# Kernel optimization log

Measured on AMD Instinct MI355X. Metric: run time of the kernel, lower is better.

## Reference

```python
import jax, jax.numpy as jnp
import numpy as np
import math

EPS = 1e-5  # torch BatchNorm2d default eps
EXPANSION_RATE = 2


def _bn_train(x, gamma, beta):
    # BatchNorm2d in training mode: biased batch statistics over (B, H, W)
    mu = jnp.mean(x, axis=(0, 2, 3), keepdims=True)
    var = jnp.var(x, axis=(0, 2, 3), keepdims=True)
    xn = (x - mu) * jax.lax.rsqrt(var + EPS)
    return gamma[None, :, None, None] * xn + beta[None, :, None, None]


def _conv1x1(x, w, b):
    # w: [O, C]  (1x1 conv kernel squeezed), b: [O]
    return jnp.einsum('bchw,oc->bohw', x, w) + b[None, :, None, None]


def _lsgc(x, w_diff, b_diff, g_bn, be_bn, w_in, b_in, g_ibn, be_ibn,
          w_mr, b_mr, g_mbn, be_mbn):
    B, C, H, W = x.shape
    bit_depth = max(math.ceil(math.log2(H)), math.ceil(math.log2(W)))
    steps = [EXPANSION_RATE * 2 ** (n - 1) for n in range(1, bit_depth + 1)]

    fmax = None
    for step in steps:
        for axis, size in ((3, W), (2, H)):
            s = step % size
            for sgn in (1, -1):  # forward / backward rolls
                shifted = jnp.roll(x, sgn * s, axis=axis) if s else x
                d = x - shifted
                fmax = d if fmax is None else jnp.maximum(fmax, d)

    x_diff = _bn_train(_conv1x1(fmax, w_diff, b_diff), g_bn, be_bn)
    x_proc = _bn_train(_conv1x1(x, w_in, b_in), g_ibn, be_ibn)

    # MRConv: concat -> 1x1 conv -> BN -> GELU (exact) -> residual add
    x_cat = jnp.concatenate([x_proc, x_diff], axis=1)
    h = _bn_train(_conv1x1(x_cat, w_mr, b_mr), g_mbn, be_mbn)
    h = jax.nn.gelu(h, approximate=False)
    return x_proc + h


def setup_inputs() -> dict:
    key = jax.random.key(0)
    ks = jax.random.split(key, 8)
    B, C_in, C_out, H, W = 32, 128, 128, 64, 64

    def kaiming(k, o, i):
        return jax.random.normal(k, (o, i), jnp.float32) * np.sqrt(2.0 / i)

    return {
        'x': jax.random.normal(ks[0], (B, C_in, H, W), jnp.float32),
        'w_diff': kaiming(ks[1], C_out, C_in),
        'b_diff': jnp.zeros((C_out,), jnp.float32),
        'g_bn': jnp.ones((C_out,), jnp.float32),
        'be_bn': jnp.zeros((C_out,), jnp.float32),
        'w_in': kaiming(ks[2], C_out, C_in),
        'b_in': jnp.zeros((C_out,), jnp.float32),
        'g_ibn': jnp.ones((C_out,), jnp.float32),
        'be_ibn': jnp.zeros((C_out,), jnp.float32),
        'w_mr': kaiming(ks[3], C_out, 2 * C_out),
        'b_mr': jnp.zeros((C_out,), jnp.float32),
        'g_mbn': jnp.ones((C_out,), jnp.float32),
        'be_mbn': jnp.zeros((C_out,), jnp.float32),
    }


def reference(x, w_diff, b_diff, g_bn, be_bn, w_in, b_in, g_ibn, be_ibn,
              w_mr, b_mr, g_mbn, be_mbn):
    return _lsgc(x, w_diff, b_diff, g_bn, be_bn, w_in, b_in, g_ibn, be_ibn,
                 w_mr, b_mr, g_mbn, be_mbn)
```

## Files before the change

### kernel.cpp

```cpp
#include <hip/hip_runtime.h>
#include <math.h>


#define INV_NPIX (1.0f / 131072.0f)
#define EPS 1e-5f
#define KP 66

typedef __attribute__((ext_vector_type(8))) short s16x8;
typedef __attribute__((ext_vector_type(4))) float f32x4;

__device__ __forceinline__ uint32_t bf16_rne(float v) {
  uint32_t x = __float_as_uint(v);
  return (x + 0x7fffu + ((x >> 16) & 1u)) >> 16;
}
__device__ __forceinline__ uint32_t pack_hl(float v) {
  uint32_t h = bf16_rne(v);
  float lo = v - __uint_as_float(h << 16);
  return h | (bf16_rne(lo) << 16);
}

__device__ __forceinline__ float4 fmin4(float4 a, float4 b) {
  return make_float4(fminf(a.x, b.x), fminf(a.y, b.y), fminf(a.z, b.z),
                     fminf(a.w, b.w));
}

__global__ __launch_bounds__(256) void stencil_prep_kernel(
    const float* __restrict__ x, float* __restrict__ out,
    const float* __restrict__ w_in, const float* __restrict__ w_diff,
    unsigned short* __restrict__ wInH, unsigned short* __restrict__ wInL,
    unsigned short* __restrict__ wDfH, unsigned short* __restrict__ wDfL,
    float* __restrict__ stats) {
  __shared__ float4 p4[1024];
  if (blockIdx.x >= 4096) {
    const int t = (blockIdx.x - 4096) * 256 + threadIdx.x;
    if (t < 24576) stats[t] = 0.f;
    const int e = t & 16383;
    const float* w = (t < 16384) ? w_in : w_diff;
    unsigned short* aH = (t < 16384) ? wInH : wDfH;
    unsigned short* aL = (t < 16384) ? wInL : wDfL;
    const int j = e & 7, l = (e >> 3) & 63, mt = (e >> 9) & 7, kc = e >> 12;
    const int m = mt * 16 + (l & 15);
    const int k = kc * 32 + ((l >> 4) << 3) + j;
    const uint32_t p = pack_hl(w[m * 128 + k]);
    aH[e] = (unsigned short)(p & 0xffffu);
    aL[e] = (unsigned short)(p >> 16);
    return;
  }
  const size_t base4 = (size_t)blockIdx.x * 1024;
  float4 self[4];
#pragma unroll
  for (int i = 0; i < 4; ++i) {
    const int u = threadIdx.x + i * 256;
    self[i] = ((const float4*)x)[base4 + u];
    p4[u] = self[i];
  }
  __syncthreads();
#pragma unroll
  for (int i = 0; i < 4; ++i) {
    const int u = threadIdx.x + i * 256;
    const int h = u >> 4, wu = u & 15;
    const int row = u & ~15;
    const float4 A = self[i];
    const float4 L = p4[row | ((wu + 15) & 15)];
    const float4 R = p4[row | ((wu + 1) & 15)];
    float4 m = A;
    m = fmin4(m, L);
    m = fmin4(m, R);
    m = fmin4(m, make_float4(A.z, A.w, R.x, R.y));
    m = fmin4(m, make_float4(L.z, L.w, A.x, A.y));
    m = fmin4(m, p4[row | ((wu + 2) & 15)]);
    m = fmin4(m, p4[row | ((wu + 14) & 15)]);
    m = fmin4(m, p4[row | ((wu + 4) & 15)]);
    m = fmin4(m, p4[row | ((wu + 12) & 15)]);
    m = fmin4(m, p4[row | ((wu + 8) & 15)]);
    m = fmin4(m, p4[(((h + 2) & 63) << 4) | wu]);
    m = fmin4(m, p4[(((h + 62) & 63) << 4) | wu]);
    m = fmin4(m, p4[(((h + 4) & 63) << 4) | wu]);
    m = fmin4(m, p4[(((h + 60) & 63) << 4) | wu]);
    m = fmin4(m, p4[(((h + 8) & 63) << 4) | wu]);
    m = fmin4(m, p4[(((h + 56) & 63) << 4) | wu]);
    m = fmin4(m, p4[(((h + 16) & 63) << 4) | wu]);
    m = fmin4(m, p4[(((h + 48) & 63) << 4) | wu]);
    m = fmin4(m, p4[(((h + 32) & 63) << 4) | wu]);
    float4 o;
    o.x = A.x - m.x;
    o.y = A.y - m.y;
    o.z = A.z - m.z;
    o.w = A.w - m.w;
    ((float4*)out)[base4 + u] = o;
  }
}

template <int K>
__device__ __forceinline__ void gemm_body(
    const unsigned short* __restrict__ AH, const unsigned short* __restrict__ AL,
    const float* __restrict__ B0, const float* __restrict__ B1,
    float* __restrict__ out, float* __restrict__ sumv,
    float* __restrict__ sumq, const int bx, uint32_t* Bs) {
  const int tid = threadIdx.x;
  const int lane = tid & 63;
  const int wave = tid >> 6;
  const int b = bx >> 6;
  const int hw0 = (bx & 63) << 6;
  const int sn4 = tid & 15;
  const int sk = tid >> 4;
  const int q = lane >> 4;
  const int ln = lane & 15;
  constexpr int NC = K / 32;

  f32x4 acc[2][4];
#pragma unroll
  for (int i = 0; i < 2; ++i)
#pragma unroll
    for (int j = 0; j < 4; ++j) acc[i][j] = (f32x4)(0.0f);

  float4 ld[4][2];
#pragma unroll
  for (int c = 0; c < 4; ++c) {
#pragma unroll
    for (int s = 0; s < 2; ++s) {
      const int kr = sk + s * 16;
      ld[c][s] = *(const float4*)&B0[((size_t)b * 128 + c * 32 + kr) * 4096 +
                                     hw0 + (sn4 << 2)];
    }
  }

#pragma unroll
  for (int kc = 0; kc < NC; ++kc) {
    const int slot = kc & 3;
    const int bsel = kc & 1;
    uint32_t* buf = Bs + bsel * (32 * KP);
#pragma unroll
    for (int s = 0; s < 2; ++s) {
      const int kr = sk + s * 16;
      uint2 d01, d23;
      d01.x = pack_hl(ld[slot][s].x);
      d01.y = pack_hl(ld[slot][s].y);
      d23.x = pack_hl(ld[slot][s].z);
      d23.y = pack_hl(ld[slot][s].w);
      *(uint2*)&buf[kr * KP + (sn4 << 2)] = d01;
      *(uint2*)&buf[kr * KP + (sn4 << 2) + 2] = d23;
    }
    s16x8 ah[2], al[2];
#pragma unroll
    for (int mt2 = 0; mt2 < 2; ++mt2) {
      const size_t off = ((size_t)((kc * 8 + wave * 2 + mt2) * 64 + lane)) << 3;
      ah[mt2] = *(const s16x8*)(AH + off);
      al[mt2] = *(const s16x8*)(AL + off);
    }
    if (K == 256 && kc < 4) {
#pragma unroll
      for (int s = 0; s < 2; ++s) {
        const int kr = sk + s * 16;
        ld[slot][s] = *(const float4*)&B1[((size_t)b * 128 + kc * 32 + kr) *
                                              4096 + hw0 + (sn4 << 2)];
      }
    }
    __syncthreads();
#pragma unroll
    for (int nt = 0; nt < 4; ++nt) {
      uint32_t dj[8];
#pragma unroll
      for (int j = 0; j < 8; ++j) dj[j] = buf[(q * 8 + j) * KP + nt * 16 + ln];
      union { uint32_t u[4]; s16x8 s; } bh, bl;
#pragma unroll
      for (int jj = 0; jj < 4; ++jj) {
        bh.u[jj] = __builtin_amdgcn_perm(dj[2 * jj + 1], dj[2 * jj], 0x05040100u);
        bl.u[jj] = __builtin_amdgcn_perm(dj[2 * jj + 1], dj[2 * jj], 0x07060302u);
      }
#pragma unroll
      for (int mt2 = 0; mt2 < 2; ++mt2) {
        acc[mt2][nt] = __builtin_amdgcn_mfma_f32_16x16x32_bf16(
            ah[mt2], bh.s, acc[mt2][nt], 0, 0, 0);
        acc[mt2][nt] = __builtin_amdgcn_mfma_f32_16x16x32_bf16(
            ah[mt2], bl.s, acc[mt2][nt], 0, 0, 0);
        acc[mt2][nt] = __builtin_amdgcn_mfma_f32_16x16x32_bf16(
            al[mt2], bh.s, acc[mt2][nt], 0, 0, 0);
      }
    }
  }

  const int cb = (bx & 31) * 128;
#pragma unroll
  for (int mt2 = 0; mt2 < 2; ++mt2) {
    float sa[4] = {0.f, 0.f, 0.f, 0.f};
    float sq[4] = {0.f, 0.f, 0.f, 0.f};
#pragma unroll
    for (int nt = 0; nt < 4; ++nt) {
#pragma unroll
      for (int r = 0; r < 4; ++r) {
        const float v = acc[mt2][nt][r];
        const int m = (wave * 2 + mt2) * 16 + q * 4 + r;
        out[((size_t)b * 128 + m) * 4096 + hw0 + nt * 16 + ln] = v;
        sa[r] += v;
        sq[r] += v * v;
      }
    }
#pragma unroll
    for (int off = 1; off < 16; off <<= 1) {
#pragma unroll
      for (int r = 0; r < 4; ++r) {
        sa[r] += __shfl_xor(sa[r], off);
        sq[r] += __shfl_xor(sq[r], off);
      }
    }
    if (ln == 0) {
#pragma unroll
      for (int r = 0; r < 4; ++r) {
        const int m = (wave * 2 + mt2) * 16 + q * 4 + r;
        atomicAdd(&sumv[cb + m], sa[r]);
        atomicAdd(&sumq[cb + m], sq[r]);
      }
    }
  }
}

__global__ __launch_bounds__(256) void gemm1_dual(
    const unsigned short* __restrict__ AH1, const unsigned short* __restrict__ AL1,
    const float* __restrict__ X, float* __restrict__ out1,
    float* __restrict__ sv1, float* __restrict__ sq1,
    const unsigned short* __restrict__ AH2, const unsigned short* __restrict__ AL2,
    const float* __restrict__ F, float* __restrict__ out2,
    float* __restrict__ sv2, float* __restrict__ sq2) {
  __shared__ uint32_t Bs[2 * 32 * KP];
  const int bx = blockIdx.x & 2047;
  if ((blockIdx.x >> 11) == 0)
    gemm_body<128>(AH1, AL1, X, nullptr, out1, sv1, sq1, bx, Bs);
  else
    gemm_body<128>(AH2, AL2, F, nullptr, out2, sv2, sq2, bx, Bs);
}

__global__ __launch_bounds__(256) void gemm2_kernel(
    const unsigned short* __restrict__ AH, const unsigned short* __restrict__ AL,
    const float* __restrict__ B0, const float* __restrict__ B1,
    float* __restrict__ out, float* __restrict__ sv, float* __restrict__ sq) {
  __shared__ uint32_t Bs[2 * 32 * KP];
  gemm_body<256>(AH, AL, B0, B1, out, sv, sq, blockIdx.x, Bs);
}

__global__ __launch_bounds__(256) void finalize1_kernel(
    const float* __restrict__ pSin, const float* __restrict__ pQin,
    const float* __restrict__ pSdf, const float* __restrict__ pQdf,
    const float* __restrict__ g_ibn, const float* __restrict__ be_ibn,
    const float* __restrict__ g_bn, const float* __restrict__ w_mr,
    float* __restrict__ a_in, float* __restrict__ d_in,
    unsigned short* __restrict__ wEffH, unsigned short* __restrict__ wEffL) {
  __shared__ float sa[256];
  const int t = threadIdx.x;
  if (t < 128) {
    float s = 0.f, qq = 0.f;
#pragma unroll
    for (int i = 0; i < 32; ++i) {
      s += pSin[i * 128 + t];
      qq += pQin[i * 128 + t];
    }
    const float mu = s * INV_NPIX;
    const float var = fmaxf(qq * INV_NPIX - mu * mu, 0.f);
    const float a = g_ibn[t] * rsqrtf(var + EPS);
    if (blockIdx.x == 0) {
      a_in[t] = a;
      d_in[t] = be_ibn[t] - mu * a;
    }
    sa[t] = a;
  } else {
    const int c = t - 128;
    float s = 0.f, qq = 0.f;
#pragma unroll
    for (int i = 0; i < 32; ++i) {
      s += pSdf[i * 128 + c];
      qq += pQdf[i * 128 + c];
    }
    const float mu = s * INV_NPIX;
    const float var = fmaxf(qq * INV_NPIX - mu * mu, 0.f);
    sa[t] = g_bn[c] * rsqrtf(var + EPS);
  }
  __syncthreads();
  const int e = blockIdx.x * 256 + t;
  const int j = e & 7, l = (e >> 3) & 63, mt = (e >> 9) & 7, kc = e >> 12;
  const int m = mt * 16 + (l & 15);
  const int k = kc * 32 + ((l >> 4) << 3) + j;
  const uint32_t p = pack_hl(w_mr[m * 256 + k] * sa[k]);
  wEffH[e] = (unsigned short)(p & 0xffffu);
  wEffL[e] = (unsigned short)(p >> 16);
}

__global__ __launch_bounds__(128) void finalize2_kernel(
    const float* __restrict__ pSh, const float* __restrict__ pQh,
    const float* __restrict__ g_mbn, const float* __restrict__ be_mbn,
    float* __restrict__ a_m, float* __restrict__ d_m) {
  const int t = threadIdx.x;
  float s = 0.f, qq = 0.f;
#pragma unroll
  for (int i = 0; i < 32; ++i) {
    s += pSh[i * 128 + t];
    qq += pQh[i * 128 + t];
  }
  const float mu = s * INV_NPIX;
  const float var = fmaxf(qq * INV_NPIX - mu * mu, 0.f);
  const float a = g_mbn[t] * rsqrtf(var + EPS);
  a_m[t] = a;
  d_m[t] = be_mbn[t] - mu * a;
}

__device__ __forceinline__ float gelu_exact(float z) {
  return 0.5f * z * (1.0f + erff(z * 0.70710678118654752f));
}

__global__ __launch_bounds__(256) void epilogue_kernel(
    const float* __restrict__ y_in, const float* __restrict__ h_pre,
    const float* __restrict__ a_in, const float* __restrict__ d_in,
    const float* __restrict__ a_m, const float* __restrict__ d_m,
    float* __restrict__ out) {
  const size_t i = (size_t)blockIdx.x * 256 + threadIdx.x;
  const int c = (int)((i >> 10) & 127);
  const float4 y = ((const float4*)y_in)[i];
  const float4 h = ((const float4*)h_pre)[i];
  const float ai = a_in[c], di = d_in[c], am = a_m[c], dm = d_m[c];
  float4 o;
  o.x = fmaf(ai, y.x, di) + gelu_exact(fmaf(am, h.x, dm));
  o.y = fmaf(ai, y.y, di) + gelu_exact(fmaf(am, h.y, dm));
  o.z = fmaf(ai, y.z, di) + gelu_exact(fmaf(am, h.z, dm));
  o.w = fmaf(ai, y.w, di) + gelu_exact(fmaf(am, h.w, dm));
  ((float4*)out)[i] = o;
}

extern "C" void kernel_launch(void* const* d_in, const int* in_sizes, int n_in,
                              void* d_out, int out_size, void* d_ws,
                              size_t ws_size, hipStream_t stream) {
  const float* x = (const float*)d_in[0];
  const float* w_diff = (const float*)d_in[1];
  const float* g_bn = (const float*)d_in[3];
  const float* w_in = (const float*)d_in[5];
  const float* g_ibn = (const float*)d_in[7];
  const float* be_ibn = (const float*)d_in[8];
  const float* w_mr = (const float*)d_in[9];
  const float* g_mbn = (const float*)d_in[11];
  const float* be_mbn = (const float*)d_in[12];
  float* out = (float*)d_out;

  const size_t NB = (size_t)16777216;
  float* ws = (float*)d_ws;
  float* buf0 = ws;
  float* buf1 = ws + NB;
  float* buf2 = ws + 2 * NB;
  float* st = ws + 3 * NB;
  float* pSin = st, *pQin = st + 4096;
  float* pSdf = st + 8192, *pQdf = st + 12288;
  float* pSh = st + 16384, *pQh = st + 20480;
  float* a_in = st + 24576, *dinc = st + 24704;
  float* a_m = st + 24832, *d_m = st + 24960;
  unsigned short* fr = (unsigned short*)(st + 25088);
  unsigned short* wInH = fr;
  unsigned short* wInL = fr + 16384;
  unsigned short* wDfH = fr + 32768;
  unsigned short* wDfL = fr + 49152;
  unsigned short* wEffH = fr + 65536;
  unsigned short* wEffL = fr + 98304;

  stencil_prep_kernel<<<4224, 256, 0, stream>>>(x, buf0, w_in, w_diff, wInH,
                                                wInL, wDfH, wDfL, st);
  gemm1_dual<<<4096, 256, 0, stream>>>(wInH, wInL, x, buf1, pSin, pQin, wDfH,
                                       wDfL, buf0, buf2, pSdf, pQdf);
  finalize1_kernel<<<128, 256, 0, stream>>>(pSin, pQin, pSdf, pQdf, g_ibn,
                                            be_ibn, g_bn, w_mr, a_in, dinc,
                                            wEffH, wEffL);
  gemm2_kernel<<<2048, 256, 0, stream>>>(wEffH, wEffL, buf1, buf2, buf0, pSh,
                                         pQh);
  finalize2_kernel<<<1, 128, 0, stream>>>(pSh, pQh, g_mbn, be_mbn, a_m, d_m);
  epilogue_kernel<<<16384, 256, 0, stream>>>(buf1, buf0, a_in, dinc, a_m, d_m,
                                             out);
}
```

Measured before the change: 276.6 us.

## Store intermediates as channel-pair-packed bf16 and drop the low-part B split

The stencil kernel now emits x and the diff map as single bf16 values, with two channels packed per 32-bit word. The GEMMs read these packed operands straight into LDS without the hi/lo split, so each step issues 2 MFMAs instead of 3. GEMM outputs and the epilogue inputs are also stored in the same packed bf16 form, which roughly halves intermediate HBM traffic. In exchange the activations lose precision (a single bf16 instead of a hi+lo pair), which risks accuracy against the fp32 reference.

```diff
diff --git a/kernel.cpp b/kernel.cpp
--- a/kernel.cpp
+++ b/kernel.cpp
@@ -18,21 +18,27 @@
   float lo = v - __uint_as_float(h << 16);
   return h | (bf16_rne(lo) << 16);
 }
-
+__device__ __forceinline__ float bf_lo(uint32_t d) {
+  return __uint_as_float(d << 16);
+}
+__device__ __forceinline__ float bf_hi(uint32_t d) {
+  return __uint_as_float(d & 0xffff0000u);
+}
 __device__ __forceinline__ float4 fmin4(float4 a, float4 b) {
   return make_float4(fminf(a.x, b.x), fminf(a.y, b.y), fminf(a.z, b.z),
                      fminf(a.w, b.w));
 }
 
 __global__ __launch_bounds__(256) void stencil_prep_kernel(
-    const float* __restrict__ x, float* __restrict__ out,
-    const float* __restrict__ w_in, const float* __restrict__ w_diff,
-    unsigned short* __restrict__ wInH, unsigned short* __restrict__ wInL,
-    unsigned short* __restrict__ wDfH, unsigned short* __restrict__ wDfL,
-    float* __restrict__ stats) {
-  __shared__ float4 p4[1024];
-  if (blockIdx.x >= 4096) {
-    const int t = (blockIdx.x - 4096) * 256 + threadIdx.x;
+    const float* __restrict__ x, uint32_t* __restrict__ xp,
+    uint32_t* __restrict__ fp, const float* __restrict__ w_in,
+    const float* __restrict__ w_diff, unsigned short* __restrict__ wInH,
+    unsigned short* __restrict__ wInL, unsigned short* __restrict__ wDfH,
+    unsigned short* __restrict__ wDfL, float* __restrict__ stats) {
+  __shared__ float4 pA[1024];
+  __shared__ float4 pB[1024];
+  if (blockIdx.x >= 2048) {
+    const int t = (blockIdx.x - 2048) * 256 + threadIdx.x;
     if (t < 24576) stats[t] = 0.f;
     const int e = t & 16383;
     const float* w = (t < 16384) ? w_in : w_diff;
@@ -46,67 +52,102 @@
     aL[e] = (unsigned short)(p >> 16);
     return;
   }
-  const size_t base4 = (size_t)blockIdx.x * 1024;
-  float4 self[4];
+  const int b = blockIdx.x >> 6;
+  const int cp = blockIdx.x & 63;
+  const float4* xa = (const float4*)x + (size_t)(b * 128 + 2 * cp) * 1024;
+  const float4* xb = xa + 1024;
+  float4 sA[4], sB[4];
 #pragma unroll
   for (int i = 0; i < 4; ++i) {
     const int u = threadIdx.x + i * 256;
-    self[i] = ((const float4*)x)[base4 + u];
-    p4[u] = self[i];
+    sA[i] = xa[u];
+    sB[i] = xb[u];
+    pA[u] = sA[i];
+    pB[u] = sB[i];
   }
   __syncthreads();
+  const size_t obase = (size_t)(b * 64 + cp) * 1024;
 #pragma unroll
   for (int i = 0; i < 4; ++i) {
     const int u = threadIdx.x + i * 256;
     const int h = u >> 4, wu = u & 15;
     const int row = u & ~15;
-    const float4 A = self[i];
-    const float4 L = p4[row | ((wu + 15) & 15)];
-    const float4 R = p4[row | ((wu + 1) & 15)];
-    float4 m = A;
-    m = fmin4(m, L);
-    m = fmin4(m, R);
-    m = fmin4(m, make_float4(A.z, A.w, R.x, R.y));
-    m = fmin4(m, make_float4(L.z, L.w, A.x, A.y));
-    m = fmin4(m, p4[row | ((wu + 2) & 15)]);
-    m = fmin4(m, p4[row | ((wu + 14) & 15)]);
-    m = fmin4(m, p4[row | ((wu + 4) & 15)]);
-    m = fmin4(m, p4[row | ((wu + 12) & 15)]);
-    m = fmin4(m, p4[row | ((wu + 8) & 15)]);
-    m = fmin4(m, p4[(((h + 2) & 63) << 4) | wu]);
-    m = fmin4(m, p4[(((h + 62) & 63) << 4) | wu]);
-    m = fmin4(m, p4[(((h + 4) & 63) << 4) | wu]);
-    m = fmin4(m, p4[(((h + 60) & 63) << 4) | wu]);
-    m = fmin4(m, p4[(((h + 8) & 63) << 4) | wu]);
-    m = fmin4(m, p4[(((h + 56) & 63) << 4) | wu]);
-    m = fmin4(m, p4[(((h + 16) & 63) << 4) | wu]);
-    m = fmin4(m, p4[(((h + 48) & 63) << 4) | wu]);
-    m = fmin4(m, p4[(((h + 32) & 63) << 4) | wu]);
-    float4 o;
-    o.x = A.x - m.x;
-    o.y = A.y - m.y;
-    o.z = A.z - m.z;
-    o.w = A.w - m.w;
-    ((float4*)out)[base4 + u] = o;
-  }
-}
-
-template <int K>
+    float4 mA, mB;
+    {
+      const float4 A = sA[i];
+      const float4 L = pA[row | ((wu + 15) & 15)];
+      const float4 R = pA[row | ((wu + 1) & 15)];
+      float4 m = fmin4(A, fmin4(L, R));
+      m = fmin4(m, make_float4(A.z, A.w, R.x, R.y));
+      m = fmin4(m, make_float4(L.z, L.w, A.x, A.y));
+      m = fmin4(m, pA[row | ((wu + 2) & 15)]);
+      m = fmin4(m, pA[row | ((wu + 14) & 15)]);
+      m = fmin4(m, pA[row | ((wu + 4) & 15)]);
+      m = fmin4(m, pA[row | ((wu + 12) & 15)]);
+      m = fmin4(m, pA[row | ((wu + 8) & 15)]);
+      m = fmin4(m, pA[(((h + 2) & 63) << 4) | wu]);
+      m = fmin4(m, pA[(((h + 62) & 63) << 4) | wu]);
+      m = fmin4(m, pA[(((h + 4) & 63) << 4) | wu]);
+      m = fmin4(m, pA[(((h + 60) & 63) << 4) | wu]);
+      m = fmin4(m, pA[(((h + 8) & 63) << 4) | wu]);
+      m = fmin4(m, pA[(((h + 56) & 63) << 4) | wu]);
+      m = fmin4(m, pA[(((h + 16) & 63) << 4) | wu]);
+      m = fmin4(m, pA[(((h + 48) & 63) << 4) | wu]);
+      m = fmin4(m, pA[(((h + 32) & 63) << 4) | wu]);
+      mA = m;
+    }
+    {
+      const float4 A = sB[i];
+      const float4 L = pB[row | ((wu + 15) & 15)];
+      const float4 R = pB[row | ((wu + 1) & 15)];
+      float4 m = fmin4(A, fmin4(L, R));
+      m = fmin4(m, make_float4(A.z, A.w, R.x, R.y));
+      m = fmin4(m, make_float4(L.z, L.w, A.x, A.y));
+      m = fmin4(m, pB[row | ((wu + 2) & 15)]);
+      m = fmin4(m, pB[row | ((wu + 14) & 15)]);
+      m = fmin4(m, pB[row | ((wu + 4) & 15)]);
+      m = fmin4(m, pB[row | ((wu + 12) & 15)]);
+      m = fmin4(m, pB[row | ((wu + 8) & 15)]);
+      m = fmin4(m, pB[(((h + 2) & 63) << 4) | wu]);
+      m = fmin4(m, pB[(((h + 62) & 63) << 4) | wu]);
+      m = fmin4(m, pB[(((h + 4) & 63) << 4) | wu]);
+      m = fmin4(m, pB[(((h + 60) & 63) << 4) | wu]);
+      m = fmin4(m, pB[(((h + 8) & 63) << 4) | wu]);
+      m = fmin4(m, pB[(((h + 56) & 63) << 4) | wu]);
+      m = fmin4(m, pB[(((h + 16) & 63) << 4) | wu]);
+      m = fmin4(m, pB[(((h + 48) & 63) << 4) | wu]);
+      m = fmin4(m, pB[(((h + 32) & 63) << 4) | wu]);
+      mB = m;
+    }
+    uint4 px, pf;
+    px.x = bf16_rne(sA[i].x) | (bf16_rne(sB[i].x) << 16);
+    px.y = bf16_rne(sA[i].y) | (bf16_rne(sB[i].y) << 16);
+    px.z = bf16_rne(sA[i].z) | (bf16_rne(sB[i].z) << 16);
+    px.w = bf16_rne(sA[i].w) | (bf16_rne(sB[i].w) << 16);
+    pf.x = bf16_rne(sA[i].x - mA.x) | (bf16_rne(sB[i].x - mB.x) << 16);
+    pf.y = bf16_rne(sA[i].y - mA.y) | (bf16_rne(sB[i].y - mB.y) << 16);
+    pf.z = bf16_rne(sA[i].z - mA.z) | (bf16_rne(sB[i].z - mB.z) << 16);
+    pf.w = bf16_rne(sA[i].w - mA.w) | (bf16_rne(sB[i].w - mB.w) << 16);
+    ((uint4*)xp)[obase + u] = px;
+    ((uint4*)fp)[obase + u] = pf;
+  }
+}
+
+template <int NC>
 __device__ __forceinline__ void gemm_body(
     const unsigned short* __restrict__ AH, const unsigned short* __restrict__ AL,
-    const float* __restrict__ B0, const float* __restrict__ B1,
-    float* __restrict__ out, float* __restrict__ sumv,
+    const uint32_t* __restrict__ B0, const uint32_t* __restrict__ B1,
+    uint32_t* __restrict__ outp, float* __restrict__ sumv,
     float* __restrict__ sumq, const int bx, uint32_t* Bs) {
   const int tid = threadIdx.x;
   const int lane = tid & 63;
   const int wave = tid >> 6;
   const int b = bx >> 6;
   const int hw0 = (bx & 63) << 6;
-  const int sn4 = tid & 15;
-  const int sk = tid >> 4;
+  const int sk2 = tid >> 4;
+  const int sn4 = (tid & 15) << 2;
   const int q = lane >> 4;
   const int ln = lane & 15;
-  constexpr int NC = K / 32;
 
   f32x4 acc[2][4];
 #pragma unroll
@@ -114,33 +155,17 @@
 #pragma unroll
     for (int j = 0; j < 4; ++j) acc[i][j] = (f32x4)(0.0f);
 
-  float4 ld[4][2];
-#pragma unroll
-  for (int c = 0; c < 4; ++c) {
-#pragma unroll
-    for (int s = 0; s < 2; ++s) {
-      const int kr = sk + s * 16;
-      ld[c][s] = *(const float4*)&B0[((size_t)b * 128 + c * 32 + kr) * 4096 +
-                                     hw0 + (sn4 << 2)];
-    }
-  }
+  uint4 ld[4];
+#pragma unroll
+  for (int c = 0; c < 4; ++c)
+    ld[c] = *(const uint4*)&B0[((size_t)(b * 64 + c * 16 + sk2)) * 4096 + hw0 +
+                               sn4];
 
 #pragma unroll
   for (int kc = 0; kc < NC; ++kc) {
     const int slot = kc & 3;
-    const int bsel = kc & 1;
-    uint32_t* buf = Bs + bsel * (32 * KP);
-#pragma unroll
-    for (int s = 0; s < 2; ++s) {
-      const int kr = sk + s * 16;
-      uint2 d01, d23;
-      d01.x = pack_hl(ld[slot][s].x);
-      d01.y = pack_hl(ld[slot][s].y);
-      d23.x = pack_hl(ld[slot][s].z);
-      d23.y = pack_hl(ld[slot][s].w);
-      *(uint2*)&buf[kr * KP + (sn4 << 2)] = d01;
-      *(uint2*)&buf[kr * KP + (sn4 << 2) + 2] = d23;
-    }
+    uint32_t* buf = Bs + (kc & 1) * (16 * KP);
+    *(uint4*)&buf[sk2 * KP + sn4] = ld[slot];
     s16x8 ah[2], al[2];
 #pragma unroll
     for (int mt2 = 0; mt2 < 2; ++mt2) {
@@ -148,34 +173,23 @@
       ah[mt2] = *(const s16x8*)(AH + off);
       al[mt2] = *(const s16x8*)(AL + off);
     }
-    if (K == 256 && kc < 4) {
-#pragma unroll
-      for (int s = 0; s < 2; ++s) {
-        const int kr = sk + s * 16;
-        ld[slot][s] = *(const float4*)&B1[((size_t)b * 128 + kc * 32 + kr) *
-                                              4096 + hw0 + (sn4 << 2)];
-      }
+    if (NC == 8 && kc < 4) {
+      ld[slot] = *(const uint4*)&B1[((size_t)(b * 64 + kc * 16 + sk2)) * 4096 +
+                                    hw0 + sn4];
     }
     __syncthreads();
 #pragma unroll
     for (int nt = 0; nt < 4; ++nt) {
-      uint32_t dj[8];
-#pragma unroll
-      for (int j = 0; j < 8; ++j) dj[j] = buf[(q * 8 + j) * KP + nt * 16 + ln];
-      union { uint32_t u[4]; s16x8 s; } bh, bl;
-#pragma unroll
-      for (int jj = 0; jj < 4; ++jj) {
-        bh.u[jj] = __builtin_amdgcn_perm(dj[2 * jj + 1], dj[2 * jj], 0x05040100u);
-        bl.u[jj] = __builtin_amdgcn_perm(dj[2 * jj + 1], dj[2 * jj], 0x07060302u);
-      }
+      union { uint32_t u[4]; s16x8 s; } bb;
+#pragma unroll
+      for (int j = 0; j < 4; ++j)
+        bb.u[j] = buf[(q * 4 + j) * KP + nt * 16 + ln];
 #pragma unroll
       for (int mt2 = 0; mt2 < 2; ++mt2) {
         acc[mt2][nt] = __builtin_amdgcn_mfma_f32_16x16x32_bf16(
-            ah[mt2], bh.s, acc[mt2][nt], 0, 0, 0);
+            ah[mt2], bb.s, acc[mt2][nt], 0, 0, 0);
         acc[mt2][nt] = __builtin_amdgcn_mfma_f32_16x16x32_bf16(
-            ah[mt2], bl.s, acc[mt2][nt], 0, 0, 0);
-        acc[mt2][nt] = __builtin_amdgcn_mfma_f32_16x16x32_bf16(
-            al[mt2], bh.s, acc[mt2][nt], 0, 0, 0);
+            al[mt2], bb.s, acc[mt2][nt], 0, 0, 0);
       }
     }
   }
@@ -188,12 +202,16 @@
 #pragma unroll
     for (int nt = 0; nt < 4; ++nt) {
 #pragma unroll
-      for (int r = 0; r < 4; ++r) {
-        const float v = acc[mt2][nt][r];
-        const int m = (wave * 2 + mt2) * 16 + q * 4 + r;
-        out[((size_t)b * 128 + m) * 4096 + hw0 + nt * 16 + ln] = v;
-        sa[r] += v;
-        sq[r] += v * v;
+      for (int rp = 0; rp < 2; ++rp) {
+        const float v0 = acc[mt2][nt][2 * rp];
+        const float v1 = acc[mt2][nt][2 * rp + 1];
+        const int m2 = (wave * 2 + mt2) * 8 + q * 2 + rp;
+        outp[((size_t)(b * 64 + m2)) * 4096 + hw0 + nt * 16 + ln] =
+            bf16_rne(v0) | (bf16_rne(v1) << 16);
+        sa[2 * rp] += v0;
+        sq[2 * rp] += v0 * v0;
+        sa[2 * rp + 1] += v1;
+        sq[2 * rp + 1] += v1 * v1;
       }
     }
 #pragma unroll
@@ -217,25 +235,26 @@
 
 __global__ __launch_bounds__(256) void gemm1_dual(
     const unsigned short* __restrict__ AH1, const unsigned short* __restrict__ AL1,
-    const float* __restrict__ X, float* __restrict__ out1,
+    const uint32_t* __restrict__ XP, uint32_t* __restrict__ out1,
     float* __restrict__ sv1, float* __restrict__ sq1,
     const unsigned short* __restrict__ AH2, const unsigned short* __restrict__ AL2,
-    const float* __restrict__ F, float* __restrict__ out2,
+    const uint32_t* __restrict__ FP, uint32_t* __restrict__ out2,
     float* __restrict__ sv2, float* __restrict__ sq2) {
-  __shared__ uint32_t Bs[2 * 32 * KP];
+  __shared__ uint32_t Bs[2 * 16 * KP];
   const int bx = blockIdx.x & 2047;
   if ((blockIdx.x >> 11) == 0)
-    gemm_body<128>(AH1, AL1, X, nullptr, out1, sv1, sq1, bx, Bs);
+    gemm_body<4>(AH1, AL1, XP, nullptr, out1, sv1, sq1, bx, Bs);
   else
-    gemm_body<128>(AH2, AL2, F, nullptr, out2, sv2, sq2, bx, Bs);
+    gemm_body<4>(AH2, AL2, FP, nullptr, out2, sv2, sq2, bx, Bs);
 }
 
 __global__ __launch_bounds__(256) void gemm2_kernel(
     const unsigned short* __restrict__ AH, const unsigned short* __restrict__ AL,
-    const float* __restrict__ B0, const float* __restrict__ B1,
-    float* __restrict__ out, float* __restrict__ sv, float* __restrict__ sq) {
-  __shared__ uint32_t Bs[2 * 32 * KP];
-  gemm_body<256>(AH, AL, B0, B1, out, sv, sq, blockIdx.x, Bs);
+    const uint32_t* __restrict__ B0, const uint32_t* __restrict__ B1,
+    uint32_t* __restrict__ outp, float* __restrict__ sv,
+    float* __restrict__ sq) {
+  __shared__ uint32_t Bs[2 * 16 * KP];
+  gemm_body<8>(AH, AL, B0, B1, outp, sv, sq, blockIdx.x, Bs);
 }
 
 __global__ __launch_bounds__(256) void finalize1_kernel(
@@ -307,21 +326,30 @@
 }
 
 __global__ __launch_bounds__(256) void epilogue_kernel(
-    const float* __restrict__ y_in, const float* __restrict__ h_pre,
+    const uint32_t* __restrict__ yp, const uint32_t* __restrict__ hp,
     const float* __restrict__ a_in, const float* __restrict__ d_in,
     const float* __restrict__ a_m, const float* __restrict__ d_m,
     float* __restrict__ out) {
   const size_t i = (size_t)blockIdx.x * 256 + threadIdx.x;
-  const int c = (int)((i >> 10) & 127);
-  const float4 y = ((const float4*)y_in)[i];
-  const float4 h = ((const float4*)h_pre)[i];
-  const float ai = a_in[c], di = d_in[c], am = a_m[c], dm = d_m[c];
-  float4 o;
-  o.x = fmaf(ai, y.x, di) + gelu_exact(fmaf(am, h.x, dm));
-  o.y = fmaf(ai, y.y, di) + gelu_exact(fmaf(am, h.y, dm));
-  o.z = fmaf(ai, y.z, di) + gelu_exact(fmaf(am, h.z, dm));
-  o.w = fmaf(ai, y.w, di) + gelu_exact(fmaf(am, h.w, dm));
-  ((float4*)out)[i] = o;
+  const int cp = (int)((i >> 10) & 63);
+  const int b = (int)(i >> 16);
+  const int c0 = 2 * cp, c1 = 2 * cp + 1;
+  const uint4 yv = ((const uint4*)yp)[i];
+  const uint4 hv = ((const uint4*)hp)[i];
+  const float a0 = a_in[c0], d0 = d_in[c0], m0 = a_m[c0], e0 = d_m[c0];
+  const float a1 = a_in[c1], d1 = d_in[c1], m1 = a_m[c1], e1 = d_m[c1];
+  float4 o0, o1;
+  o0.x = fmaf(a0, bf_lo(yv.x), d0) + gelu_exact(fmaf(m0, bf_lo(hv.x), e0));
+  o0.y = fmaf(a0, bf_lo(yv.y), d0) + gelu_exact(fmaf(m0, bf_lo(hv.y), e0));
+  o0.z = fmaf(a0, bf_lo(yv.z), d0) + gelu_exact(fmaf(m0, bf_lo(hv.z), e0));
+  o0.w = fmaf(a0, bf_lo(yv.w), d0) + gelu_exact(fmaf(m0, bf_lo(hv.w), e0));
+  o1.x = fmaf(a1, bf_hi(yv.x), d1) + gelu_exact(fmaf(m1, bf_hi(hv.x), e1));
+  o1.y = fmaf(a1, bf_hi(yv.y), d1) + gelu_exact(fmaf(m1, bf_hi(hv.y), e1));
+  o1.z = fmaf(a1, bf_hi(yv.z), d1) + gelu_exact(fmaf(m1, bf_hi(hv.z), e1));
+  o1.w = fmaf(a1, bf_hi(yv.w), d1) + gelu_exact(fmaf(m1, bf_hi(hv.w), e1));
+  const size_t u = i & 1023;
+  ((float4*)out)[(size_t)(b * 128 + c0) * 1024 + u] = o0;
+  ((float4*)out)[(size_t)(b * 128 + c1) * 1024 + u] = o1;
 }
 
 extern "C" void kernel_launch(void* const* d_in, const int* in_sizes, int n_in,
@@ -338,12 +366,14 @@
   const float* be_mbn = (const float*)d_in[12];
   float* out = (float*)d_out;
 
-  const size_t NB = (size_t)16777216;
-  float* ws = (float*)d_ws;
-  float* buf0 = ws;
-  float* buf1 = ws + NB;
-  float* buf2 = ws + 2 * NB;
-  float* st = ws + 3 * NB;
+  const size_t PD = (size_t)8388608;
+  uint32_t* ws = (uint32_t*)d_ws;
+  uint32_t* xp = ws;
+  uint32_t* fpx = ws + PD;
+  uint32_t* ypIn = ws + 2 * PD;
+  uint32_t* ypDf = ws + 3 * PD;
+  uint32_t* hp = ws + 4 * PD;
+  float* st = (float*)(ws + 5 * PD);
   float* pSin = st, *pQin = st + 4096;
   float* pSdf = st + 8192, *pQdf = st + 12288;
   float* pSh = st + 16384, *pQh = st + 20480;
@@ -357,16 +387,16 @@
   unsigned short* wEffH = fr + 65536;
   unsigned short* wEffL = fr + 98304;
 
-  stencil_prep_kernel<<<4224, 256, 0, stream>>>(x, buf0, w_in, w_diff, wInH,
-                                                wInL, wDfH, wDfL, st);
-  gemm1_dual<<<4096, 256, 0, stream>>>(wInH, wInL, x, buf1, pSin, pQin, wDfH,
-                                       wDfL, buf0, buf2, pSdf, pQdf);
+  stencil_prep_kernel<<<2176, 256, 0, stream>>>(x, xp, fpx, w_in, w_diff,
+                                                wInH, wInL, wDfH, wDfL, st);
+  gemm1_dual<<<4096, 256, 0, stream>>>(wInH, wInL, xp, ypIn, pSin, pQin, wDfH,
+                                       wDfL, fpx, ypDf, pSdf, pQdf);
   finalize1_kernel<<<128, 256, 0, stream>>>(pSin, pQin, pSdf, pQdf, g_ibn,
                                             be_ibn, g_bn, w_mr, a_in, dinc,
                                             wEffH, wEffL);
-  gemm2_kernel<<<2048, 256, 0, stream>>>(wEffH, wEffL, buf1, buf2, buf0, pSh,
+  gemm2_kernel<<<2048, 256, 0, stream>>>(wEffH, wEffL, ypIn, ypDf, hp, pSh,
                                          pQh);
   finalize2_kernel<<<1, 128, 0, stream>>>(pSh, pQh, g_mbn, be_mbn, a_m, d_m);
-  epilogue_kernel<<<16384, 256, 0, stream>>>(buf1, buf0, a_in, dinc, a_m, d_m,
-                                             out);
-}
+  epilogue_kernel<<<8192, 256, 0, stream>>>(ypIn, hp, a_in, dinc, a_m, d_m,
+                                            out);
+}
```

Result: no change. 271.2 us (-2.0%).
